# Kernel tuning notes

Measured on AMD Instinct MI355X. Metric: run time of the kernel, lower is better.

Reference implementation:

```python
import jax, jax.numpy as jnp
import numpy as np

N_ENT = 50000   # entities (nodes)
N_REL = 500     # relations
DEG = 32        # regular in-degree of the full KG
TOPK = 10       # topk in-edges kept per node by dgl.sampling.select_topk
H_DIM = 256
N_HEADS = 4
HEAD_DIM = H_DIM // N_HEADS
NEG_SLOPE = 0.2


def _leaky(x):
    return jnp.where(x >= 0, x, NEG_SLOPE * x)


def setup_inputs() -> dict:
    key = jax.random.key(0)
    ks = jax.random.split(key, 8)
    s = 0.05
    return {
        'ent_emb': jax.random.normal(ks[0], (N_ENT, H_DIM), dtype=jnp.float32),
        'rel_emb': jax.random.normal(ks[1], (N_REL, H_DIM), dtype=jnp.float32),
        'W': jax.random.normal(ks[2], (N_HEADS, H_DIM, HEAD_DIM), dtype=jnp.float32) * s,
        'W_r': jax.random.normal(ks[3], (N_HEADS, H_DIM, HEAD_DIM), dtype=jnp.float32) * s,
        'a': jax.random.normal(ks[4], (N_HEADS, 3 * HEAD_DIM), dtype=jnp.float32) * s,
        'neigh_w': jax.random.normal(ks[5], (H_DIM, H_DIM), dtype=jnp.float32) * s,
        'src': jax.random.randint(ks[6], (N_ENT, DEG), 0, N_ENT),   # src node of each in-edge of node n
        'rel_id': jax.random.randint(ks[7], (N_ENT, DEG), 0, N_REL),
    }


def reference(ent_emb, rel_emb, W, W_r, a, neigh_w, src, rel_id):
    # ---- head-0 scores used for top-k in-edge sampling (select_topk, edge_dir='in') ----
    emb_t0 = ent_emb @ W[0]          # [N, hd]
    rel_t0 = rel_emb @ W_r[0]        # [R, hd]
    a0 = a[0]
    # concat([src,dst,rel]) @ a  ==  src@a_src + dst@a_dst + rel@a_rel
    s_src = emb_t0 @ a0[:HEAD_DIM]                 # [N]
    s_dst = emb_t0 @ a0[HEAD_DIM:2 * HEAD_DIM]     # [N]
    s_rel = rel_t0 @ a0[2 * HEAD_DIM:]             # [R]
    score0 = _leaky(s_src[src] + s_dst[:, None] + s_rel[rel_id])   # [N, DEG]
    _, top_idx = jax.lax.top_k(score0, TOPK)                        # [N, K]
    src_sel = jnp.take_along_axis(src, top_idx, axis=1)             # [N, K]
    rel_sel = jnp.take_along_axis(rel_id, top_idx, axis=1)          # [N, K]

    # ---- all heads on the sampled subgraph (vectorized over heads) ----
    emb_t = jnp.einsum('nd,hde->hne', ent_emb, W)     # [H, N, hd]
    rel_t = jnp.einsum('rd,hde->hre', rel_emb, W_r)   # [H, R, hd]
    a3 = a.reshape(N_HEADS, 3, HEAD_DIM)
    ss = jnp.einsum('hne,he->hn', emb_t, a3[:, 0])    # [H, N]
    sd = jnp.einsum('hne,he->hn', emb_t, a3[:, 1])    # [H, N]
    sr = jnp.einsum('hre,he->hr', rel_t, a3[:, 2])    # [H, R]
    scores = _leaky(ss[:, src_sel] + sd[:, :, None] + sr[:, rel_sel])  # [H, N, K]
    norm = jax.nn.softmax(scores, axis=-1)            # edge-softmax over in-edges per dst

    # comp_op == 'add' : u_add_e, weighted by attention, summed into dst
    comp = emb_t[:, src_sel] + rel_t[:, rel_sel]      # [H, N, K, hd]
    neigh = jnp.einsum('hnke,hnk->hne', comp, norm)   # [H, N, hd]

    neigh = jnp.transpose(neigh, (1, 0, 2)).reshape(ent_emb.shape[0], H_DIM)  # concat heads
    return jnp.tanh(neigh @ neigh_w)                  # bn disabled (cfg.bn=False)
```

## Files before the change

kernel.cpp:

```cpp
#include <hip/hip_runtime.h>
#include <math.h>

#define N_ENT 50000
#define N_REL 500
#define DEG 32
#define TOPK 10
#define H_DIM 256
#define N_HEADS 4
#define HEAD_DIM 64

typedef __attribute__((ext_vector_type(8))) short short8v;
typedef __attribute__((ext_vector_type(4))) float f32x4;

constexpr size_t OFF_SSRC0 = 0;
constexpr size_t OFF_SR0   = 400000;
constexpr size_t OFF_U0    = 404000;
constexpr size_t OFF_V0    = 406048;
constexpr size_t OFF_SS    = 408096;
constexpr size_t OFF_SSR   = 2008096;
constexpr size_t OFF_U8    = 2024096;
constexpr size_t OFF_V8    = 2032288;
constexpr size_t OFF_B1H   = 2040480;
constexpr size_t OFF_B2H   = 2302624;
constexpr size_t OFF_B3H   = 2564768;
constexpr size_t OFF_NPK   = 3089056;
constexpr size_t OFF_EMBBF = 28713632;
constexpr size_t OFF_RELBF = 54313632;
constexpr size_t WS_NEED   = 54569632;

__device__ __forceinline__ float leaky(float x) { return x >= 0.f ? x : 0.2f * x; }

__device__ __forceinline__ unsigned short bf16_rne(float x) {
    unsigned int u = __float_as_uint(x);
    unsigned int r = u + 0x7fffu + ((u >> 16) & 1u);
    return (unsigned short)(r >> 16);
}
__device__ __forceinline__ float bf2f(unsigned short x) {
    return __uint_as_float((unsigned)x << 16);
}

__device__ __forceinline__ size_t pack_off(int row, int d) {
    return ((size_t)(row >> 4) * 8 + (d >> 5)) * 512 +
           (((d >> 3) & 3) * 16 + (row & 15)) * 8 + (d & 7);
}

__global__ __launch_bounds__(256) void setup_kernel(
    const float* __restrict__ W, const float* __restrict__ W_r,
    const float* __restrict__ a, const float* __restrict__ nw,
    float* __restrict__ U8, double* __restrict__ u0,
    float* __restrict__ V8, double* __restrict__ v0,
    unsigned short* __restrict__ b1h, unsigned short* __restrict__ b2h,
    unsigned short* __restrict__ b3h)
{
    const int bid = blockIdx.x;
    const int tid = threadIdx.x;
    if (bid == 0) {
        int d = tid;
        #pragma unroll
        for (int h = 0; h < N_HEADS; ++h) {
            float ss = 0.f, sd = 0.f;
            #pragma unroll
            for (int e = 0; e < HEAD_DIM; ++e) {
                float w = W[h * 16384 + d * 64 + e];
                ss += w * a[h * 192 + e];
                sd += w * a[h * 192 + 64 + e];
            }
            U8[d * 8 + h] = ss;
            U8[d * 8 + 4 + h] = sd;
        }
        double s0 = 0.0;
        #pragma unroll
        for (int e = 0; e < HEAD_DIM; ++e)
            s0 += (double)W[d * 64 + e] * (double)a[e];
        u0[d] = s0;
    } else if (bid == 1) {
        int d = tid;
        #pragma unroll
        for (int h = 0; h < N_HEADS; ++h) {
            float sv = 0.f;
            #pragma unroll
            for (int e = 0; e < HEAD_DIM; ++e)
                sv += W_r[h * 16384 + d * 64 + e] * a[h * 192 + 128 + e];
            V8[d * 8 + h] = sv;
            V8[d * 8 + 4 + h] = 0.f;
        }
        double s0 = 0.0;
        #pragma unroll
        for (int e = 0; e < HEAD_DIM; ++e)
            s0 += (double)W_r[d * 64 + e] * (double)a[128 + e];
        v0[d] = s0;
    } else {
        int n = bid - 2;
        int k = tid;
        int h = n >> 6, e = n & 63;
        float x1 = W[h * 16384 + k * 64 + e];
        float x2 = nw[k * 256 + n];
        float x3 = W_r[h * 16384 + k * 64 + e];
        size_t off = pack_off(n, k);
        b1h[off] = bf16_rne(x1);
        b2h[off] = bf16_rne(x2);
        b3h[off] = bf16_rne(x3);
    }
}

__global__ __launch_bounds__(256) void mid_kernel(
    const float* __restrict__ ent, const float* __restrict__ relm,
    const unsigned short* __restrict__ b1h, const unsigned short* __restrict__ b3h,
    unsigned short* __restrict__ embbf, unsigned short* __restrict__ relbf,
    const float* __restrict__ U8, const double* __restrict__ u0,
    const float* __restrict__ V8, const double* __restrict__ v0,
    float* __restrict__ SS, double* __restrict__ ssrc0,
    float* __restrict__ SSR, double* __restrict__ sr0)
{
    __shared__ unsigned short As[64][264];

    const int b = blockIdx.x;
    const int tid = threadIdx.x;
    const int l = tid & 63;
    const int el = l & 31;

    if (b < 790) {
        const int w = tid >> 6;
        const int rl = l & 15;
        const int ql = l >> 4;

        const bool isent = (b < 782);
        const float* Af = isent ? ent : relm;
        const unsigned short* Bh = isent ? b1h : b3h;
        unsigned short* C = isent ? embbf : relbf;
        const int M = isent ? N_ENT : N_REL;
        const int bm = (isent ? b : (b - 782)) * 64;

        #pragma unroll
        for (int i = 0; i < 8; ++i) {
            int u = i * 256 + tid;
            int row = u >> 5;
            int c8 = (u & 31) * 8;
            int grow = min(bm + row, M - 1);
            float4 v1 = *(const float4*)(Af + (size_t)grow * 256 + c8);
            float4 v2 = *(const float4*)(Af + (size_t)grow * 256 + c8 + 4);
            short8v ov;
            ov[0] = (short)bf16_rne(v1.x); ov[1] = (short)bf16_rne(v1.y);
            ov[2] = (short)bf16_rne(v1.z); ov[3] = (short)bf16_rne(v1.w);
            ov[4] = (short)bf16_rne(v2.x); ov[5] = (short)bf16_rne(v2.y);
            ov[6] = (short)bf16_rne(v2.z); ov[7] = (short)bf16_rne(v2.w);
            *(short8v*)&As[row][c8] = ov;
        }
        __syncthreads();

        const unsigned short* bhb = Bh + (size_t)w * 16384 + l * 8;

        f32x4 acc[4][4];
        #pragma unroll
        for (int i = 0; i < 4; ++i)
            #pragma unroll
            for (int j = 0; j < 4; ++j) acc[i][j] = (f32x4){0.f, 0.f, 0.f, 0.f};

        #pragma unroll
        for (int ks = 0; ks < 8; ++ks) {
            short8v ah[4], bh[4];
            #pragma unroll
            for (int mf = 0; mf < 4; ++mf)
                ah[mf] = *(const short8v*)&As[mf * 16 + rl][ks * 32 + ql * 8];
            #pragma unroll
            for (int nf = 0; nf < 4; ++nf)
                bh[nf] = *(const short8v*)(bhb + nf * 4096 + ks * 512);
            #pragma unroll
            for (int mf = 0; mf < 4; ++mf)
                #pragma unroll
                for (int nf = 0; nf < 4; ++nf)
                    acc[mf][nf] = __builtin_amdgcn_mfma_f32_16x16x32_bf16(ah[mf], bh[nf], acc[mf][nf], 0, 0, 0);
        }

        #pragma unroll
        for (int mf = 0; mf < 4; ++mf) {
            int row0 = bm + mf * 16 + ql * 4;
            #pragma unroll
            for (int nf = 0; nf < 4; ++nf) {
                int c = w * 64 + nf * 16 + rl;
                #pragma unroll
                for (int j = 0; j < 4; ++j) {
                    int r = row0 + j;
                    if (r < M)
                        C[(size_t)r * 256 + c] = bf16_rne(acc[mf][nf][j]);
                }
            }
        }
    } else {
        const int q2 = l >> 5;
        const bool isent = (b < 2838);
        const float* X = isent ? ent : relm;
        const float* U8v = isent ? U8 : V8;
        const double* u0v = isent ? u0 : v0;
        float* SSout = isent ? SS : SSR;
        double* s0out = isent ? ssrc0 : sr0;
        const int N = isent ? N_ENT : N_REL;
        const int wave0 = isent ? (((b - 790) * 256 + tid) >> 6)
                                : (((b - 2838) * 256 + tid) >> 6);
        const int nwaves = isent ? 8192 : 252;

        float uu[8][8];
        #pragma unroll
        for (int i = 0; i < 8; ++i) {
            float4 a4 = *(const float4*)(U8v + (el * 8 + i) * 8);
            float4 b4 = *(const float4*)(U8v + (el * 8 + i) * 8 + 4);
            uu[i][0] = a4.x; uu[i][1] = a4.y; uu[i][2] = a4.z; uu[i][3] = a4.w;
            uu[i][4] = b4.x; uu[i][5] = b4.y; uu[i][6] = b4.z; uu[i][7] = b4.w;
        }
        double ud[8];
        #pragma unroll
        for (int i = 0; i < 8; ++i) ud[i] = u0v[el * 8 + i];

        const int jout = ((el & 1) << 2) | (el & 2) | ((el >> 2) & 1);
        const int half = N / 2;

        int p = wave0;
        float4 x1, x2;
        if (p < half) {
            int n0 = p * 2 + q2;
            x1 = *(const float4*)(X + (size_t)n0 * 256 + el * 8);
            x2 = *(const float4*)(X + (size_t)n0 * 256 + el * 8 + 4);
        }
        for (; p < half; p += nwaves) {
            const int n = p * 2 + q2;
            const float4 cx1 = x1, cx2 = x2;
            const int np = p + nwaves;
            if (np < half) {
                int n1 = np * 2 + q2;
                x1 = *(const float4*)(X + (size_t)n1 * 256 + el * 8);
                x2 = *(const float4*)(X + (size_t)n1 * 256 + el * 8 + 4);
            }
            float xs[8] = {cx1.x, cx1.y, cx1.z, cx1.w, cx2.x, cx2.y, cx2.z, cx2.w};

            float pj[8] = {0.f, 0.f, 0.f, 0.f, 0.f, 0.f, 0.f, 0.f};
            double pd = 0.0;
            #pragma unroll
            for (int i = 0; i < 8; ++i) {
                #pragma unroll
                for (int j = 0; j < 8; ++j) pj[j] += xs[i] * uu[i][j];
                pd += (double)xs[i] * ud[i];
            }

            const bool b1 = (el & 1);
            float q[4];
            #pragma unroll
            for (int j = 0; j < 4; ++j) {
                float mine = b1 ? pj[j + 4] : pj[j];
                float send = b1 ? pj[j] : pj[j + 4];
                q[j] = mine + __shfl_xor(send, 1);
            }
            const bool b2 = (el & 2);
            float r2[2];
            #pragma unroll
            for (int j = 0; j < 2; ++j) {
                float mine = b2 ? q[j + 2] : q[j];
                float send = b2 ? q[j] : q[j + 2];
                r2[j] = mine + __shfl_xor(send, 2);
            }
            const bool b4 = (el & 4);
            {
                float mine = b4 ? r2[1] : r2[0];
                float send = b4 ? r2[0] : r2[1];
                r2[0] = mine + __shfl_xor(send, 4);
            }
            r2[0] += __shfl_xor(r2[0], 8);
            r2[0] += __shfl_xor(r2[0], 16);

            #pragma unroll
            for (int off = 1; off < 32; off <<= 1) pd += __shfl_xor(pd, off);

            if (el < 8) SSout[(size_t)n * 8 + jout] = r2[0];
            if (el == 0) s0out[n] = pd;
        }
    }
}

__global__ __launch_bounds__(256, 3) void node_kernel(
    const int* __restrict__ src, const int* __restrict__ relid,
    const float* __restrict__ SS, const double* __restrict__ ssrc0,
    const float* __restrict__ SSR, const double* __restrict__ sr0,
    const unsigned short* __restrict__ emb_bf, const unsigned short* __restrict__ rel_bf,
    unsigned short* __restrict__ napk)
{
    __shared__ double scs[8][33];
    __shared__ unsigned idsS[8][12];
    __shared__ float wtsS[8][10][4];
    __shared__ float sumsS[8][4];

    const int tid = threadIdx.x;
    const int l = tid & 63;
    const int el = l & 31;
    const int hb = l & 32;
    const int nib = tid >> 5;
    const int n = blockIdx.x * 8 + nib;

    const int sd_ = src[n * DEG + el];
    const int rd_ = relid[n * DEG + el];
    const double sc0 = ssrc0[sd_] + sr0[rd_];
    scs[nib][el] = sc0;

    int cnt = 0;
    #pragma unroll
    for (int j = 0; j < DEG; ++j) {
        double sj = scs[nib][j];
        cnt += (sj > sc0 || (sj == sc0 && j < el)) ? 1 : 0;
    }
    const bool sel = (cnt < TOPK);
    const unsigned mask = (unsigned)(__ballot(sel) >> hb);
    const int pos = __popc(mask & ((1u << el) - 1u));

    float ex = 0.f, ey = 0.f, ez = 0.f, ew = 0.f;
    if (sel) {
        float4 ssv = *(const float4*)(SS + (size_t)sd_ * 8);
        float4 srv = *(const float4*)(SSR + (size_t)rd_ * 8);
        float4 sdv = *(const float4*)(SS + (size_t)n * 8 + 4);
        ex = __expf(leaky(ssv.x + sdv.x + srv.x));
        ey = __expf(leaky(ssv.y + sdv.y + srv.y));
        ez = __expf(leaky(ssv.z + sdv.z + srv.z));
        ew = __expf(leaky(ssv.w + sdv.w + srv.w));
        idsS[nib][pos] = (unsigned)sd_ | ((unsigned)rd_ << 16);
        float4 wv; wv.x = ex; wv.y = ey; wv.z = ez; wv.w = ew;
        *(float4*)&wtsS[nib][pos][0] = wv;
    }

    float p0, p1;
    {
        const bool b1 = (el & 1);
        float m0 = b1 ? ez : ex, s0 = b1 ? ex : ez;
        float m1 = b1 ? ew : ey, s1 = b1 ? ey : ew;
        p0 = m0 + __shfl_xor(s0, 1);
        p1 = m1 + __shfl_xor(s1, 1);
    }
    float qsum;
    {
        const bool b2 = (el & 2);
        float m = b2 ? p1 : p0, s = b2 ? p0 : p1;
        qsum = m + __shfl_xor(s, 2);
    }
    qsum += __shfl_xor(qsum, 4);
    qsum += __shfl_xor(qsum, 8);
    qsum += __shfl_xor(qsum, 16);
    if (el < 4) sumsS[nib][((el & 1) << 1) | ((el >> 1) & 1)] = qsum;

    const int h = el >> 3;

    int skA[TOPK], rkA[TOPK];
    #pragma unroll
    for (int k = 0; k < TOPK; ++k) {
        unsigned idk = idsS[nib][k];
        skA[k] = (int)(idk & 0xFFFFu);
        rkA[k] = (int)(idk >> 16);
    }

    short8v ev[TOPK], rv[TOPK];
    #pragma unroll
    for (int k = 0; k < TOPK; ++k)
        ev[k] = *(const short8v*)(emb_bf + (size_t)skA[k] * 256 + el * 8);
    #pragma unroll
    for (int k = 0; k < TOPK; ++k)
        rv[k] = *(const short8v*)(rel_bf + (size_t)rkA[k] * 256 + el * 8);
    asm volatile("s_waitcnt vmcnt(0)" ::: "memory");

    const float rsh = 1.f / sumsS[nib][h];
    float acc[8] = {0.f, 0.f, 0.f, 0.f, 0.f, 0.f, 0.f, 0.f};
    #pragma unroll
    for (int k = 0; k < TOPK; ++k) {
        float w = wtsS[nib][k][h] * rsh;
        #pragma unroll
        for (int j = 0; j < 8; ++j)
            acc[j] += w * (bf2f((unsigned short)ev[k][j]) + bf2f((unsigned short)rv[k][j]));
    }

    short8v ov;
    #pragma unroll
    for (int j = 0; j < 8; ++j) ov[j] = (short)bf16_rne(acc[j]);
    *(short8v*)(napk + (size_t)n * 256 + el * 8) = ov;
}

__global__ __launch_bounds__(256, 4) void gemm_out(
    const unsigned short* __restrict__ A, const unsigned short* __restrict__ Bpkh,
    float* __restrict__ Cout, int M)
{
    __shared__ unsigned short As[64][264];

    const int tid = threadIdx.x;
    const int l = tid & 63;
    const int w = tid >> 6;
    const int bm = blockIdx.x * 64;
    const int rl = l & 15;
    const int ql = l >> 4;

    const unsigned short* Ag = A + (size_t)bm * 256;
    #pragma unroll
    for (int i = 0; i < 8; ++i) {
        int u = i * 256 + tid;
        short8v v = *(const short8v*)(Ag + (size_t)u * 8);
        *(short8v*)&As[u >> 5][(u & 31) * 8] = v;
    }
    __syncthreads();

    const unsigned short* bhb = Bpkh + (size_t)w * 16384 + l * 8;

    f32x4 acc[4][4];
    #pragma unroll
    for (int i = 0; i < 4; ++i)
        #pragma unroll
        for (int j = 0; j < 4; ++j) acc[i][j] = (f32x4){0.f, 0.f, 0.f, 0.f};

    #pragma unroll
    for (int ks = 0; ks < 8; ++ks) {
        short8v ah[4], bh[4];
        #pragma unroll
        for (int mf = 0; mf < 4; ++mf)
            ah[mf] = *(const short8v*)&As[mf * 16 + rl][ks * 32 + ql * 8];
        #pragma unroll
        for (int nf = 0; nf < 4; ++nf)
            bh[nf] = *(const short8v*)(bhb + nf * 4096 + ks * 512);
        #pragma unroll
        for (int mf = 0; mf < 4; ++mf)
            #pragma unroll
            for (int nf = 0; nf < 4; ++nf)
                acc[mf][nf] = __builtin_amdgcn_mfma_f32_16x16x32_bf16(ah[mf], bh[nf], acc[mf][nf], 0, 0, 0);
    }

    #pragma unroll
    for (int mf = 0; mf < 4; ++mf) {
        int row0 = bm + mf * 16 + ql * 4;
        #pragma unroll
        for (int nf = 0; nf < 4; ++nf) {
            int c = w * 64 + nf * 16 + rl;
            #pragma unroll
            for (int j = 0; j < 4; ++j) {
                int r = row0 + j;
                if (r < M) {
                    float v = acc[mf][nf][j];
                    Cout[(size_t)r * 256 + c] = 1.f - 2.f / (__expf(2.f * v) + 1.f);
                }
            }
        }
    }
}

extern "C" void kernel_launch(void* const* d_in, const int* in_sizes, int n_in,
                              void* d_out, int out_size, void* d_ws, size_t ws_size,
                              hipStream_t stream) {
    const float* ent  = (const float*)d_in[0];
    const float* rel  = (const float*)d_in[1];
    const float* W    = (const float*)d_in[2];
    const float* W_r  = (const float*)d_in[3];
    const float* a    = (const float*)d_in[4];
    const float* nw   = (const float*)d_in[5];
    const int*   srcp = (const int*)d_in[6];
    const int*   ridp = (const int*)d_in[7];
    float* out = (float*)d_out;

    if (ws_size < WS_NEED) return;

    char* ws = (char*)d_ws;
    double* ssrc0 = (double*)(ws + OFF_SSRC0);
    double* sr0   = (double*)(ws + OFF_SR0);
    double* u0    = (double*)(ws + OFF_U0);
    double* v0    = (double*)(ws + OFF_V0);
    float*  SS    = (float*)(ws + OFF_SS);
    float*  SSR   = (float*)(ws + OFF_SSR);
    float*  U8    = (float*)(ws + OFF_U8);
    float*  V8    = (float*)(ws + OFF_V8);
    unsigned short* b1h = (unsigned short*)(ws + OFF_B1H);
    unsigned short* b2h = (unsigned short*)(ws + OFF_B2H);
    unsigned short* b3h = (unsigned short*)(ws + OFF_B3H);
    unsigned short* napk = (unsigned short*)(ws + OFF_NPK);
    unsigned short* embbf = (unsigned short*)(ws + OFF_EMBBF);
    unsigned short* relbf = (unsigned short*)(ws + OFF_RELBF);

    setup_kernel<<<258, 256, 0, stream>>>(W, W_r, a, nw, U8, u0, V8, v0,
                                          b1h, b2h, b3h);
    mid_kernel<<<2901, 256, 0, stream>>>(ent, rel, b1h, b3h, embbf, relbf,
                                         U8, u0, V8, v0, SS, ssrc0, SSR, sr0);
    node_kernel<<<6250, 256, 0, stream>>>(srcp, ridp, SS, ssrc0, SSR, sr0,
                                          embbf, relbf, napk);
    gemm_out<<<782, 256, 0, stream>>>(napk, b2h, out, N_ENT);
}
```

Measured before the change: 138.9 us.

## Fuse score projection into GEMM tile load so entity rows are read once

```diff
diff --git a/kernel.cpp b/kernel.cpp
--- a/kernel.cpp
+++ b/kernel.cpp
@@ -103,7 +103,7 @@
     }
 }
 
-__global__ __launch_bounds__(256) void mid_kernel(
+__global__ __launch_bounds__(256, 3) void mid_kernel(
     const float* __restrict__ ent, const float* __restrict__ relm,
     const unsigned short* __restrict__ b1h, const unsigned short* __restrict__ b3h,
     unsigned short* __restrict__ embbf, unsigned short* __restrict__ relbf,
@@ -118,159 +118,127 @@
     const int tid = threadIdx.x;
     const int l = tid & 63;
     const int el = l & 31;
-
-    if (b < 790) {
-        const int w = tid >> 6;
-        const int rl = l & 15;
-        const int ql = l >> 4;
-
-        const bool isent = (b < 782);
-        const float* Af = isent ? ent : relm;
-        const unsigned short* Bh = isent ? b1h : b3h;
-        unsigned short* C = isent ? embbf : relbf;
-        const int M = isent ? N_ENT : N_REL;
-        const int bm = (isent ? b : (b - 782)) * 64;
-
-        #pragma unroll
-        for (int i = 0; i < 8; ++i) {
-            int u = i * 256 + tid;
-            int row = u >> 5;
-            int c8 = (u & 31) * 8;
-            int grow = min(bm + row, M - 1);
-            float4 v1 = *(const float4*)(Af + (size_t)grow * 256 + c8);
-            float4 v2 = *(const float4*)(Af + (size_t)grow * 256 + c8 + 4);
-            short8v ov;
-            ov[0] = (short)bf16_rne(v1.x); ov[1] = (short)bf16_rne(v1.y);
-            ov[2] = (short)bf16_rne(v1.z); ov[3] = (short)bf16_rne(v1.w);
-            ov[4] = (short)bf16_rne(v2.x); ov[5] = (short)bf16_rne(v2.y);
-            ov[6] = (short)bf16_rne(v2.z); ov[7] = (short)bf16_rne(v2.w);
-            *(short8v*)&As[row][c8] = ov;
-        }
-        __syncthreads();
-
-        const unsigned short* bhb = Bh + (size_t)w * 16384 + l * 8;
-
-        f32x4 acc[4][4];
-        #pragma unroll
-        for (int i = 0; i < 4; ++i)
-            #pragma unroll
-            for (int j = 0; j < 4; ++j) acc[i][j] = (f32x4){0.f, 0.f, 0.f, 0.f};
-
-        #pragma unroll
-        for (int ks = 0; ks < 8; ++ks) {
-            short8v ah[4], bh[4];
-            #pragma unroll
-            for (int mf = 0; mf < 4; ++mf)
-                ah[mf] = *(const short8v*)&As[mf * 16 + rl][ks * 32 + ql * 8];
+    const int w = tid >> 6;
+    const int rl = l & 15;
+    const int ql = l >> 4;
+
+    const bool isent = (b < 782);
+    const float* Af = isent ? ent : relm;
+    const unsigned short* Bh = isent ? b1h : b3h;
+    unsigned short* C = isent ? embbf : relbf;
+    const float* U8v = isent ? U8 : V8;
+    const double* u0v = isent ? u0 : v0;
+    float* SSout = isent ? SS : SSR;
+    double* s0out = isent ? ssrc0 : sr0;
+    const int M = isent ? N_ENT : N_REL;
+    const int bm = (isent ? b : (b - 782)) * 64;
+
+    float uu[8][8];
+    #pragma unroll
+    for (int i = 0; i < 8; ++i) {
+        float4 a4 = *(const float4*)(U8v + (el * 8 + i) * 8);
+        float4 b4 = *(const float4*)(U8v + (el * 8 + i) * 8 + 4);
+        uu[i][0] = a4.x; uu[i][1] = a4.y; uu[i][2] = a4.z; uu[i][3] = a4.w;
+        uu[i][4] = b4.x; uu[i][5] = b4.y; uu[i][6] = b4.z; uu[i][7] = b4.w;
+    }
+    double ud[8];
+    #pragma unroll
+    for (int i = 0; i < 8; ++i) ud[i] = u0v[el * 8 + i];
+
+    const int jout = ((el & 1) << 2) | (el & 2) | ((el >> 2) & 1);
+
+    #pragma unroll
+    for (int i = 0; i < 8; ++i) {
+        const int row = i * 8 + (tid >> 5);
+        const int grow = min(bm + row, M - 1);
+        const float* rp = Af + (size_t)grow * 256 + el * 8;
+        float4 v1 = *(const float4*)(rp);
+        float4 v2 = *(const float4*)(rp + 4);
+        float xs[8] = {v1.x, v1.y, v1.z, v1.w, v2.x, v2.y, v2.z, v2.w};
+
+        short8v ov;
+        #pragma unroll
+        for (int j = 0; j < 8; ++j) ov[j] = (short)bf16_rne(xs[j]);
+        *(short8v*)&As[row][el * 8] = ov;
+
+        float pj[8] = {0.f, 0.f, 0.f, 0.f, 0.f, 0.f, 0.f, 0.f};
+        double pd = 0.0;
+        #pragma unroll
+        for (int ii = 0; ii < 8; ++ii) {
+            #pragma unroll
+            for (int j = 0; j < 8; ++j) pj[j] += xs[ii] * uu[ii][j];
+            pd += (double)xs[ii] * ud[ii];
+        }
+
+        const bool b1 = (el & 1);
+        float q[4];
+        #pragma unroll
+        for (int j = 0; j < 4; ++j) {
+            float mine = b1 ? pj[j + 4] : pj[j];
+            float send = b1 ? pj[j] : pj[j + 4];
+            q[j] = mine + __shfl_xor(send, 1);
+        }
+        const bool b2 = (el & 2);
+        float r2[2];
+        #pragma unroll
+        for (int j = 0; j < 2; ++j) {
+            float mine = b2 ? q[j + 2] : q[j];
+            float send = b2 ? q[j] : q[j + 2];
+            r2[j] = mine + __shfl_xor(send, 2);
+        }
+        const bool b4 = (el & 4);
+        {
+            float mine = b4 ? r2[1] : r2[0];
+            float send = b4 ? r2[0] : r2[1];
+            r2[0] = mine + __shfl_xor(send, 4);
+        }
+        r2[0] += __shfl_xor(r2[0], 8);
+        r2[0] += __shfl_xor(r2[0], 16);
+
+        #pragma unroll
+        for (int off = 1; off < 32; off <<= 1) pd += __shfl_xor(pd, off);
+
+        if (el < 8) SSout[(size_t)grow * 8 + jout] = r2[0];
+        if (el == 0) s0out[grow] = pd;
+    }
+    __syncthreads();
+
+    const unsigned short* bhb = Bh + (size_t)w * 16384 + l * 8;
+
+    f32x4 acc[4][4];
+    #pragma unroll
+    for (int i = 0; i < 4; ++i)
+        #pragma unroll
+        for (int j = 0; j < 4; ++j) acc[i][j] = (f32x4){0.f, 0.f, 0.f, 0.f};
+
+    #pragma unroll
+    for (int ks = 0; ks < 8; ++ks) {
+        short8v ah[4], bh[4];
+        #pragma unroll
+        for (int mf = 0; mf < 4; ++mf)
+            ah[mf] = *(const short8v*)&As[mf * 16 + rl][ks * 32 + ql * 8];
+        #pragma unroll
+        for (int nf = 0; nf < 4; ++nf)
+            bh[nf] = *(const short8v*)(bhb + nf * 4096 + ks * 512);
+        #pragma unroll
+        for (int mf = 0; mf < 4; ++mf)
             #pragma unroll
             for (int nf = 0; nf < 4; ++nf)
-                bh[nf] = *(const short8v*)(bhb + nf * 4096 + ks * 512);
-            #pragma unroll
-            for (int mf = 0; mf < 4; ++mf)
-                #pragma unroll
-                for (int nf = 0; nf < 4; ++nf)
-                    acc[mf][nf] = __builtin_amdgcn_mfma_f32_16x16x32_bf16(ah[mf], bh[nf], acc[mf][nf], 0, 0, 0);
-        }
-
-        #pragma unroll
-        for (int mf = 0; mf < 4; ++mf) {
-            int row0 = bm + mf * 16 + ql * 4;
-            #pragma unroll
-            for (int nf = 0; nf < 4; ++nf) {
-                int c = w * 64 + nf * 16 + rl;
-                #pragma unroll
-                for (int j = 0; j < 4; ++j) {
-                    int r = row0 + j;
-                    if (r < M)
-                        C[(size_t)r * 256 + c] = bf16_rne(acc[mf][nf][j]);
-                }
+                acc[mf][nf] = __builtin_amdgcn_mfma_f32_16x16x32_bf16(ah[mf], bh[nf], acc[mf][nf], 0, 0, 0);
+    }
+
+    #pragma unroll
+    for (int mf = 0; mf < 4; ++mf) {
+        int row0 = bm + mf * 16 + ql * 4;
+        #pragma unroll
+        for (int nf = 0; nf < 4; ++nf) {
+            int c = w * 64 + nf * 16 + rl;
+            #pragma unroll
+            for (int j = 0; j < 4; ++j) {
+                int r = row0 + j;
+                if (r < M)
+                    C[(size_t)r * 256 + c] = bf16_rne(acc[mf][nf][j]);
             }
-        }
-    } else {
-        const int q2 = l >> 5;
-        const bool isent = (b < 2838);
-        const float* X = isent ? ent : relm;
-        const float* U8v = isent ? U8 : V8;
-        const double* u0v = isent ? u0 : v0;
-        float* SSout = isent ? SS : SSR;
-        double* s0out = isent ? ssrc0 : sr0;
-        const int N = isent ? N_ENT : N_REL;
-        const int wave0 = isent ? (((b - 790) * 256 + tid) >> 6)
-                                : (((b - 2838) * 256 + tid) >> 6);
-        const int nwaves = isent ? 8192 : 252;
-
-        float uu[8][8];
-        #pragma unroll
-        for (int i = 0; i < 8; ++i) {
-            float4 a4 = *(const float4*)(U8v + (el * 8 + i) * 8);
-            float4 b4 = *(const float4*)(U8v + (el * 8 + i) * 8 + 4);
-            uu[i][0] = a4.x; uu[i][1] = a4.y; uu[i][2] = a4.z; uu[i][3] = a4.w;
-            uu[i][4] = b4.x; uu[i][5] = b4.y; uu[i][6] = b4.z; uu[i][7] = b4.w;
-        }
-        double ud[8];
-        #pragma unroll
-        for (int i = 0; i < 8; ++i) ud[i] = u0v[el * 8 + i];
-
-        const int jout = ((el & 1) << 2) | (el & 2) | ((el >> 2) & 1);
-        const int half = N / 2;
-
-        int p = wave0;
-        float4 x1, x2;
-        if (p < half) {
-            int n0 = p * 2 + q2;
-            x1 = *(const float4*)(X + (size_t)n0 * 256 + el * 8);
-            x2 = *(const float4*)(X + (size_t)n0 * 256 + el * 8 + 4);
-        }
-        for (; p < half; p += nwaves) {
-            const int n = p * 2 + q2;
-            const float4 cx1 = x1, cx2 = x2;
-            const int np = p + nwaves;
-            if (np < half) {
-                int n1 = np * 2 + q2;
-                x1 = *(const float4*)(X + (size_t)n1 * 256 + el * 8);
-                x2 = *(const float4*)(X + (size_t)n1 * 256 + el * 8 + 4);
-            }
-            float xs[8] = {cx1.x, cx1.y, cx1.z, cx1.w, cx2.x, cx2.y, cx2.z, cx2.w};
-
-            float pj[8] = {0.f, 0.f, 0.f, 0.f, 0.f, 0.f, 0.f, 0.f};
-            double pd = 0.0;
-            #pragma unroll
-            for (int i = 0; i < 8; ++i) {
-                #pragma unroll
-                for (int j = 0; j < 8; ++j) pj[j] += xs[i] * uu[i][j];
-                pd += (double)xs[i] * ud[i];
-            }
-
-            const bool b1 = (el & 1);
-            float q[4];
-            #pragma unroll
-            for (int j = 0; j < 4; ++j) {
-                float mine = b1 ? pj[j + 4] : pj[j];
-                float send = b1 ? pj[j] : pj[j + 4];
-                q[j] = mine + __shfl_xor(send, 1);
-            }
-            const bool b2 = (el & 2);
-            float r2[2];
-            #pragma unroll
-            for (int j = 0; j < 2; ++j) {
-                float mine = b2 ? q[j + 2] : q[j];
-                float send = b2 ? q[j] : q[j + 2];
-                r2[j] = mine + __shfl_xor(send, 2);
-            }
-            const bool b4 = (el & 4);
-            {
-                float mine = b4 ? r2[1] : r2[0];
-                float send = b4 ? r2[0] : r2[1];
-                r2[0] = mine + __shfl_xor(send, 4);
-            }
-            r2[0] += __shfl_xor(r2[0], 8);
-            r2[0] += __shfl_xor(r2[0], 16);
-
-            #pragma unroll
-            for (int off = 1; off < 32; off <<= 1) pd += __shfl_xor(pd, off);
-
-            if (el < 8) SSout[(size_t)n * 8 + jout] = r2[0];
-            if (el == 0) s0out[n] = pd;
         }
     }
 }
@@ -474,8 +442,8 @@
 
     setup_kernel<<<258, 256, 0, stream>>>(W, W_r, a, nw, U8, u0, V8, v0,
                                           b1h, b2h, b3h);
-    mid_kernel<<<2901, 256, 0, stream>>>(ent, rel, b1h, b3h, embbf, relbf,
-                                         U8, u0, V8, v0, SS, ssrc0, SSR, sr0);
+    mid_kernel<<<790, 256, 0, stream>>>(ent, rel, b1h, b3h, embbf, relbf,
+                                        U8, u0, V8, v0, SS, ssrc0, SSR, sr0);
     node_kernel<<<6250, 256, 0, stream>>>(srcp, ridp, SS, ssrc0, SSR, sr0,
                                           embbf, relbf, napk);
     gemm_out<<<782, 256, 0, stream>>>(napk, b2h, out, N_ENT);
```

Measured after the change: 125.0 us, median of 2. -10.0%, faster.
